# Kernel optimization log

Measured on AMD Instinct MI355X. Metric: run time of the kernel, lower is better.

## Reference

```python
import jax, jax.numpy as jnp
import numpy as np

CHEB_K = 3  # diffusion_steps

def setup_inputs() -> dict:
    key = jax.random.key(0)
    k1, k2, k3 = jax.random.split(key, 3)
    N, D, B, C, O, K = 2048, 16, 64, 64, 64, CHEB_K
    node_embeddings = jax.random.normal(k1, (N, D), dtype=jnp.float32)
    feat = jax.random.normal(k2, (B, N, C), dtype=jnp.float32)
    # kaiming-uniform-like init for weights_pool, zeros bias (matches reset_parameters)
    fan_in = K * C  # fan_in of [D, K, C, O] per torch convention (dims after first)
    bound = 1.0 / np.sqrt(fan_in)
    weights_pool = jax.random.uniform(k3, (D, K, C, O), dtype=jnp.float32,
                                      minval=-bound, maxval=bound)
    bias_pool = jnp.zeros((D, O), dtype=jnp.float32)
    return {"node_embeddings": node_embeddings, "feat": feat,
            "weights_pool": weights_pool, "bias_pool": bias_pool}

def reference(node_embeddings, feat, weights_pool, bias_pool):
    N = node_embeddings.shape[0]
    K = weights_pool.shape[1]
    # adaptive adjacency: softmax(relu(E E^T)) row-wise
    sim = node_embeddings @ node_embeddings.T            # [N, N]
    supports = jax.nn.softmax(jax.nn.relu(sim), axis=1)  # [N, N]
    # Chebyshev polynomial recurrence: T0=I, T1=A, Tk = 2A Tk-1 - Tk-2
    support_set = [jnp.eye(N, dtype=supports.dtype), supports]
    for _ in range(2, K):
        support_set.append(2.0 * supports @ support_set[-1] - support_set[-2])
    supports_k = jnp.stack(support_set, axis=0)          # [K, N, N]
    # node-conditioned weights and bias
    weights = jnp.einsum('nd,dkio->nkio', node_embeddings, weights_pool)  # [N,K,C,O]
    bias = node_embeddings @ bias_pool                                    # [N, O]
    # graph diffusion of features
    x_g = jnp.einsum('knm,bmc->bknc', supports_k, feat)  # [B, K, N, C]
    x_g = jnp.transpose(x_g, (0, 2, 1, 3))               # [B, N, K, C]
    # per-node batched GEMM + bias
    x_gconv = jnp.einsum('bnki,nkio->bno', x_g, weights) + bias
    return x_gconv
```

## Files before the change

### kernel.cpp

```cpp
#include <hip/hip_runtime.h>
#include <stdint.h>

#define NN 2048
#define DE 16
#define BB 64
#define CC 64
#define OO 64
#define BC 4096
#define KR 192

using bf16x8 = __attribute__((ext_vector_type(8))) __bf16;
using f32x4  = __attribute__((ext_vector_type(4))) float;

__device__ __forceinline__ unsigned short f2bf(float f) {
  union { float f; unsigned int u; } v; v.f = f;
  unsigned int u = v.u;
  return (unsigned short)((u + 0x7FFFu + ((u >> 16) & 1u)) >> 16);
}
__device__ __forceinline__ float bf2f(unsigned short h) {
  union { unsigned int u; float f; } v; v.u = ((unsigned int)h) << 16;
  return v.f;
}
__device__ __forceinline__ void gll16(const void* g, void* l) {
  __builtin_amdgcn_global_load_lds(
      (const __attribute__((address_space(1))) unsigned int*)g,
      (__attribute__((address_space(3))) unsigned int*)l, 16, 0, 0);
}

__global__ __launch_bounds__(256) void pack_feat(const float* __restrict__ feat,
                                                 unsigned short* __restrict__ Fbf,
                                                 unsigned short* __restrict__ FbfT) {
  __shared__ float tile[64][65];
  const int b  = blockIdx.y;
  const int n0 = blockIdx.x * 64;
  const int t  = threadIdx.x;
  const int tr = t >> 4, tc4 = (t & 15) * 4;
#pragma unroll
  for (int i = 0; i < 4; ++i) {
    const int r = tr + i * 16;
    const float4 v = *(const float4*)(feat + (size_t)b * (NN * CC) + (size_t)(n0 + r) * CC + tc4);
    tile[r][tc4 + 0] = v.x; tile[r][tc4 + 1] = v.y;
    tile[r][tc4 + 2] = v.z; tile[r][tc4 + 3] = v.w;
  }
  __syncthreads();
#pragma unroll
  for (int i = 0; i < 4; ++i) {
    const int r = tr + i * 16;
    const unsigned int lo = f2bf(tile[r][tc4 + 0]) | ((unsigned int)f2bf(tile[r][tc4 + 1]) << 16);
    const unsigned int hi = f2bf(tile[r][tc4 + 2]) | ((unsigned int)f2bf(tile[r][tc4 + 3]) << 16);
    *(uint2*)(Fbf + (size_t)(n0 + r) * BC + b * CC + tc4) = make_uint2(lo, hi);
  }
  const int rr = t & 63;
  const int cb = t >> 6;
#pragma unroll
  for (int i = 0; i < 16; ++i) {
    const int c = cb * 16 + i;
    FbfT[(size_t)(b * CC + c) * NN + n0 + rr] = f2bf(tile[rr][c]);
  }
}

__global__ __launch_bounds__(256) void adj_softmax(const float* __restrict__ E,
                                                   const float* __restrict__ bias_pool,
                                                   unsigned short* __restrict__ Abf,
                                                   float* __restrict__ Bias) {
  const int n = blockIdx.x, t = threadIdx.x;
  __shared__ float en[16];
  __shared__ float red[8];
  if (t < 16) en[t] = E[n * 16 + t];
  __syncthreads();
  float er[16];
#pragma unroll
  for (int d = 0; d < 16; ++d) er[d] = en[d];

  float v[8];
  float mx = 0.0f;
#pragma unroll
  for (int i = 0; i < 8; ++i) {
    const int m = t + i * 256;
    const float4* Em = (const float4*)(E + m * 16);
    const float4 a = Em[0], b = Em[1], c = Em[2], d = Em[3];
    float dot = er[0] * a.x + er[1] * a.y + er[2] * a.z + er[3] * a.w
              + er[4] * b.x + er[5] * b.y + er[6] * b.z + er[7] * b.w
              + er[8] * c.x + er[9] * c.y + er[10] * c.z + er[11] * c.w
              + er[12] * d.x + er[13] * d.y + er[14] * d.z + er[15] * d.w;
    v[i] = fmaxf(dot, 0.0f);
    mx = fmaxf(mx, v[i]);
  }
#pragma unroll
  for (int off = 32; off > 0; off >>= 1) mx = fmaxf(mx, __shfl_xor(mx, off, 64));
  const int wave = t >> 6, lane = t & 63;
  if (lane == 0) red[wave] = mx;
  __syncthreads();
  mx = fmaxf(fmaxf(red[0], red[1]), fmaxf(red[2], red[3]));
  float s = 0.0f;
#pragma unroll
  for (int i = 0; i < 8; ++i) { v[i] = __expf(v[i] - mx); s += v[i]; }
#pragma unroll
  for (int off = 32; off > 0; off >>= 1) s += __shfl_xor(s, off, 64);
  if (lane == 0) red[4 + wave] = s;
  __syncthreads();
  s = red[4] + red[5] + red[6] + red[7];
  const float inv = 1.0f / s;
#pragma unroll
  for (int i = 0; i < 8; ++i)
    Abf[(size_t)n * NN + t + i * 256] = f2bf(v[i] * inv);
  if (t < 64) {
    float bs = 0.0f;
#pragma unroll
    for (int d = 0; d < 16; ++d) bs += er[d] * bias_pool[d * 64 + t];
    Bias[n * 64 + t] = bs;
  }
}

__global__ __launch_bounds__(256) void make_w(const float* __restrict__ wp,
                                              const float* __restrict__ E,
                                              unsigned short* __restrict__ Wg) {
  __shared__ float wl[16][8][64];
  __shared__ float el[64][16];
  const int rq = blockIdx.x;
  const int n0 = blockIdx.y * 64;
  const int t  = threadIdx.x;
  for (int p = t; p < 2048; p += 256) {
    const int idx = p * 4;
    const int d = idx >> 9, rem = idx & 511, rl = rem >> 6, o = rem & 63;
    *(float4*)&wl[d][rl][o] = *(const float4*)(wp + (size_t)d * (KR * OO) + (size_t)(rq * 8 + rl) * 64 + o);
  }
  {
    const int nl = t >> 2, d4 = (t & 3) * 4;
    *(float4*)&el[nl][d4] = *(const float4*)(E + (size_t)(n0 + nl) * 16 + d4);
  }
  __syncthreads();
  const int o = t & 63, ng = t >> 6;
  for (int ii = 0; ii < 16; ++ii) {
    const int nl = ng * 16 + ii;
    float a[8] = {0, 0, 0, 0, 0, 0, 0, 0};
#pragma unroll
    for (int d = 0; d < 16; ++d) {
      const float e = el[nl][d];
#pragma unroll
      for (int rl = 0; rl < 8; ++rl) a[rl] = fmaf(e, wl[d][rl][o], a[rl]);
    }
    const unsigned int w0 = f2bf(a[0]) | ((unsigned int)f2bf(a[1]) << 16);
    const unsigned int w1 = f2bf(a[2]) | ((unsigned int)f2bf(a[3]) << 16);
    const unsigned int w2 = f2bf(a[4]) | ((unsigned int)f2bf(a[5]) << 16);
    const unsigned int w3 = f2bf(a[6]) | ((unsigned int)f2bf(a[7]) << 16);
    *(uint4*)(Wg + (size_t)(n0 + nl) * (KR * OO) + (size_t)rq * 512 + o * 8) =
        make_uint4(w0, w1, w2, w3);
  }
}

template <int EPI>
__global__ __launch_bounds__(256, 2) void gemm128(const unsigned short* __restrict__ A,
                                                  const unsigned short* __restrict__ Bt,
                                                  unsigned short* __restrict__ Cnm,
                                                  unsigned short* __restrict__ Ct,
                                                  const unsigned short* __restrict__ F) {
  __shared__ alignas(16) unsigned short As[128 * 32];
  __shared__ alignas(16) unsigned short Bs[128 * 32];
  const int t = threadIdx.x;
  const int bm = blockIdx.y * 128, bn = blockIdx.x * 128;
  const int wave = t >> 6, lane = t & 63;
  const int wm = (wave >> 1) * 64, wn = (wave & 1) * 64;

  f32x4 acc[4][4];
#pragma unroll
  for (int r = 0; r < 4; ++r)
#pragma unroll
    for (int c = 0; c < 4; ++c) acc[r][c] = (f32x4){0.f, 0.f, 0.f, 0.f};

  const int e0 = t * 8, e1 = (t + 256) * 8;
  const int r0 = e0 >> 5, c0 = e0 & 31;
  const int r1 = e1 >> 5, c1 = e1 & 31;
  const unsigned short* A0 = A + (size_t)(bm + r0) * NN + c0;
  const unsigned short* A1 = A + (size_t)(bm + r1) * NN + c1;
  const unsigned short* B0 = Bt + (size_t)(bn + r0) * NN + c0;
  const unsigned short* B1 = Bt + (size_t)(bn + r1) * NN + c1;
  const int aoff = (wm + (lane & 15)) * 32 + (lane >> 4) * 8;
  const int boff = (wn + (lane & 15)) * 32 + (lane >> 4) * 8;

  for (int k0 = 0; k0 < NN; k0 += 32) {
    __syncthreads();
    gll16(A0 + k0, &As[e0]);
    gll16(A1 + k0, &As[e1]);
    gll16(B0 + k0, &Bs[e0]);
    gll16(B1 + k0, &Bs[e1]);
    __syncthreads();
    bf16x8 af[4], bfr[4];
#pragma unroll
    for (int r = 0; r < 4; ++r) af[r] = *(const bf16x8*)&As[aoff + r * 512];
#pragma unroll
    for (int c = 0; c < 4; ++c) bfr[c] = *(const bf16x8*)&Bs[boff + c * 512];
#pragma unroll
    for (int r = 0; r < 4; ++r)
#pragma unroll
      for (int c = 0; c < 4; ++c)
        acc[r][c] = __builtin_amdgcn_mfma_f32_16x16x32_bf16(af[r], bfr[c], acc[r][c], 0, 0, 0);
  }

  const int colL = lane & 15, rowL = (lane >> 4) * 4;
#pragma unroll
  for (int r = 0; r < 4; ++r) {
#pragma unroll
    for (int c = 0; c < 4; ++c) {
      const int gm = bm + wm + r * 16 + rowL;
      const int gn = bn + wn + c * 16 + colL;
      const f32x4 a = acc[r][c];
      if (EPI == 1) {
#pragma unroll
        for (int i = 0; i < 4; ++i)
          Cnm[(size_t)(gm + i) * BC + gn] = f2bf(a[i]);
        const unsigned int lo = f2bf(a[0]) | ((unsigned int)f2bf(a[1]) << 16);
        const unsigned int hi = f2bf(a[2]) | ((unsigned int)f2bf(a[3]) << 16);
        *(uint2*)(Ct + (size_t)gn * NN + gm) = make_uint2(lo, hi);
      } else {
#pragma unroll
        for (int i = 0; i < 4; ++i) {
          const float g = 2.0f * a[i] - bf2f(F[(size_t)(gm + i) * BC + gn]);
          Cnm[(size_t)(gm + i) * BC + gn] = f2bf(g);
        }
      }
    }
  }
}

__global__ __launch_bounds__(256) void final_gemm(const unsigned short* __restrict__ Fbf,
                                                  const unsigned short* __restrict__ G1,
                                                  const unsigned short* __restrict__ G2,
                                                  const unsigned short* __restrict__ Wg,
                                                  const float* __restrict__ Bias,
                                                  float* __restrict__ out) {
  __shared__ alignas(16) unsigned short Xl[64 * 200];
  __shared__ alignas(16) unsigned short Wl[KR * OO];
  const int n = blockIdx.x, t = threadIdx.x;
  const unsigned short* srcs[3] = {Fbf + (size_t)n * BC, G1 + (size_t)n * BC, G2 + (size_t)n * BC};
#pragma unroll
  for (int kk = 0; kk < 3; ++kk) {
    const uint4* s = (const uint4*)srcs[kk];
    for (int p = t; p < 512; p += 256) {
      const uint4 v = s[p];
      const int j = p * 8, b = j >> 6, i = j & 63;
      *(uint4*)&Xl[b * 200 + kk * 64 + i] = v;
    }
  }
  {
    const uint4* s = (const uint4*)(Wg + (size_t)n * (KR * OO));
    uint4* d = (uint4*)Wl;
    for (int p = t; p < 1536; p += 256) d[p] = s[p];
  }
  __syncthreads();

  const int wave = t >> 6, lane = t & 63;
  const int q = lane >> 4;
  const int brow = wave * 16 + (lane & 15);
  f32x4 acc[4];
#pragma unroll
  for (int c = 0; c < 4; ++c) acc[c] = (f32x4){0.f, 0.f, 0.f, 0.f};
#pragma unroll
  for (int kq = 0; kq < 6; ++kq) {
    const bf16x8 a = *(const bf16x8*)&Xl[brow * 200 + kq * 32 + q * 8];
#pragma unroll
    for (int c = 0; c < 4; ++c) {
      const bf16x8 b = *(const bf16x8*)&Wl[(kq * 4 + q) * 512 + (c * 16 + (lane & 15)) * 8];
      acc[c] = __builtin_amdgcn_mfma_f32_16x16x32_bf16(a, b, acc[c], 0, 0, 0);
    }
  }
  const int col = lane & 15, rbase = wave * 16 + q * 4;
#pragma unroll
  for (int c = 0; c < 4; ++c) {
    const int o = c * 16 + col;
    const float bs = Bias[n * 64 + o];
#pragma unroll
    for (int i = 0; i < 4; ++i)
      out[(size_t)(rbase + i) * (NN * OO) + (size_t)n * OO + o] = acc[c][i] + bs;
  }
}

extern "C" void kernel_launch(void* const* d_in, const int* in_sizes, int n_in,
                              void* d_out, int out_size, void* d_ws, size_t ws_size,
                              hipStream_t stream) {
  const float* E    = (const float*)d_in[0];
  const float* feat = (const float*)d_in[1];
  const float* wp   = (const float*)d_in[2];
  const float* bp   = (const float*)d_in[3];
  float* out = (float*)d_out;

  char* ws = (char*)d_ws;
  size_t off = 0;
  auto alloc = [&](size_t bytes) -> void* {
    void* p = ws + off;
    off += (bytes + 255) & ~(size_t)255;
    return p;
  };
  unsigned short* Abf  = (unsigned short*)alloc((size_t)NN * NN * 2);
  unsigned short* FbfT = (unsigned short*)alloc((size_t)BC * NN * 2);
  unsigned short* Fbf  = (unsigned short*)alloc((size_t)NN * BC * 2);
  unsigned short* G1   = (unsigned short*)alloc((size_t)NN * BC * 2);
  unsigned short* G1T  = (unsigned short*)alloc((size_t)BC * NN * 2);
  unsigned short* Wg   = (unsigned short*)alloc((size_t)NN * KR * OO * 2);
  float* Bias          = (float*)alloc((size_t)NN * OO * 4);
  unsigned short* G2   = FbfT;

  pack_feat<<<dim3(32, 64), 256, 0, stream>>>(feat, Fbf, FbfT);
  adj_softmax<<<dim3(2048), 256, 0, stream>>>(E, bp, Abf, Bias);
  make_w<<<dim3(24, 32), 256, 0, stream>>>(wp, E, Wg);
  gemm128<1><<<dim3(32, 16), 256, 0, stream>>>(Abf, FbfT, G1, G1T, nullptr);
  gemm128<2><<<dim3(32, 16), 256, 0, stream>>>(Abf, G1T, G2, nullptr, Fbf);
  final_gemm<<<dim3(2048), 256, 0, stream>>>(Fbf, G1, G2, Wg, Bias, out);
}
```

Before: 256.6 us.

## Merge prep kernels into one launch, restructure weight gen, swizzle GEMM LDS

Combines the feature pack, adjacency softmax and per-node weight generation into a single block-indexed prep kernel, so two launches and their tail gaps go away. Weight generation now keeps the pool weights in registers and streams node embeddings through scalar loads instead of staging both in shared memory. Separately, the GEMM LDS tiles use an XOR swizzle on the 8-element column chunk to reduce bank conflicts on fragment reads. The fused kernel's occupancy is bounded by its largest branch's shared memory and register use, and the weight branch holds a 64-float register array.

Measured after the change: 239.7 us. -6.6%, faster.

```diff
diff --git a/kernel.cpp b/kernel.cpp
--- a/kernel.cpp
+++ b/kernel.cpp
@@ -27,125 +27,124 @@
       (__attribute__((address_space(3))) unsigned int*)l, 16, 0, 0);
 }
 
-__global__ __launch_bounds__(256) void pack_feat(const float* __restrict__ feat,
-                                                 unsigned short* __restrict__ Fbf,
-                                                 unsigned short* __restrict__ FbfT) {
-  __shared__ float tile[64][65];
-  const int b  = blockIdx.y;
-  const int n0 = blockIdx.x * 64;
+__global__ __launch_bounds__(256) void prep(const float* __restrict__ feat,
+                                            const float* __restrict__ E,
+                                            const float* __restrict__ wp,
+                                            const float* __restrict__ bp,
+                                            unsigned short* __restrict__ Fbf,
+                                            unsigned short* __restrict__ FbfT,
+                                            unsigned short* __restrict__ Abf,
+                                            float* __restrict__ Bias,
+                                            unsigned short* __restrict__ Wg) {
+  __shared__ float smem[64 * 65];
+  const int id = blockIdx.x;
   const int t  = threadIdx.x;
-  const int tr = t >> 4, tc4 = (t & 15) * 4;
-#pragma unroll
-  for (int i = 0; i < 4; ++i) {
-    const int r = tr + i * 16;
-    const float4 v = *(const float4*)(feat + (size_t)b * (NN * CC) + (size_t)(n0 + r) * CC + tc4);
-    tile[r][tc4 + 0] = v.x; tile[r][tc4 + 1] = v.y;
-    tile[r][tc4 + 2] = v.z; tile[r][tc4 + 3] = v.w;
-  }
-  __syncthreads();
-#pragma unroll
-  for (int i = 0; i < 4; ++i) {
-    const int r = tr + i * 16;
-    const unsigned int lo = f2bf(tile[r][tc4 + 0]) | ((unsigned int)f2bf(tile[r][tc4 + 1]) << 16);
-    const unsigned int hi = f2bf(tile[r][tc4 + 2]) | ((unsigned int)f2bf(tile[r][tc4 + 3]) << 16);
-    *(uint2*)(Fbf + (size_t)(n0 + r) * BC + b * CC + tc4) = make_uint2(lo, hi);
-  }
-  const int rr = t & 63;
-  const int cb = t >> 6;
-#pragma unroll
-  for (int i = 0; i < 16; ++i) {
-    const int c = cb * 16 + i;
-    FbfT[(size_t)(b * CC + c) * NN + n0 + rr] = f2bf(tile[rr][c]);
-  }
-}
-
-__global__ __launch_bounds__(256) void adj_softmax(const float* __restrict__ E,
-                                                   const float* __restrict__ bias_pool,
-                                                   unsigned short* __restrict__ Abf,
-                                                   float* __restrict__ Bias) {
-  const int n = blockIdx.x, t = threadIdx.x;
-  __shared__ float en[16];
-  __shared__ float red[8];
-  if (t < 16) en[t] = E[n * 16 + t];
-  __syncthreads();
-  float er[16];
-#pragma unroll
-  for (int d = 0; d < 16; ++d) er[d] = en[d];
-
-  float v[8];
-  float mx = 0.0f;
-#pragma unroll
-  for (int i = 0; i < 8; ++i) {
-    const int m = t + i * 256;
-    const float4* Em = (const float4*)(E + m * 16);
-    const float4 a = Em[0], b = Em[1], c = Em[2], d = Em[3];
-    float dot = er[0] * a.x + er[1] * a.y + er[2] * a.z + er[3] * a.w
-              + er[4] * b.x + er[5] * b.y + er[6] * b.z + er[7] * b.w
-              + er[8] * c.x + er[9] * c.y + er[10] * c.z + er[11] * c.w
-              + er[12] * d.x + er[13] * d.y + er[14] * d.z + er[15] * d.w;
-    v[i] = fmaxf(dot, 0.0f);
-    mx = fmaxf(mx, v[i]);
-  }
-#pragma unroll
-  for (int off = 32; off > 0; off >>= 1) mx = fmaxf(mx, __shfl_xor(mx, off, 64));
-  const int wave = t >> 6, lane = t & 63;
-  if (lane == 0) red[wave] = mx;
-  __syncthreads();
-  mx = fmaxf(fmaxf(red[0], red[1]), fmaxf(red[2], red[3]));
-  float s = 0.0f;
-#pragma unroll
-  for (int i = 0; i < 8; ++i) { v[i] = __expf(v[i] - mx); s += v[i]; }
-#pragma unroll
-  for (int off = 32; off > 0; off >>= 1) s += __shfl_xor(s, off, 64);
-  if (lane == 0) red[4 + wave] = s;
-  __syncthreads();
-  s = red[4] + red[5] + red[6] + red[7];
-  const float inv = 1.0f / s;
-#pragma unroll
-  for (int i = 0; i < 8; ++i)
-    Abf[(size_t)n * NN + t + i * 256] = f2bf(v[i] * inv);
-  if (t < 64) {
-    float bs = 0.0f;
-#pragma unroll
-    for (int d = 0; d < 16; ++d) bs += er[d] * bias_pool[d * 64 + t];
-    Bias[n * 64 + t] = bs;
-  }
-}
-
-__global__ __launch_bounds__(256) void make_w(const float* __restrict__ wp,
-                                              const float* __restrict__ E,
-                                              unsigned short* __restrict__ Wg) {
-  __shared__ float wl[16][8][64];
-  __shared__ float el[64][16];
-  const int rq = blockIdx.x;
-  const int n0 = blockIdx.y * 64;
-  const int t  = threadIdx.x;
-  for (int p = t; p < 2048; p += 256) {
-    const int idx = p * 4;
-    const int d = idx >> 9, rem = idx & 511, rl = rem >> 6, o = rem & 63;
-    *(float4*)&wl[d][rl][o] = *(const float4*)(wp + (size_t)d * (KR * OO) + (size_t)(rq * 8 + rl) * 64 + o);
-  }
-  {
-    const int nl = t >> 2, d4 = (t & 3) * 4;
-    *(float4*)&el[nl][d4] = *(const float4*)(E + (size_t)(n0 + nl) * 16 + d4);
-  }
-  __syncthreads();
-  const int o = t & 63, ng = t >> 6;
-  for (int ii = 0; ii < 16; ++ii) {
-    const int nl = ng * 16 + ii;
-    float a[8] = {0, 0, 0, 0, 0, 0, 0, 0};
-#pragma unroll
-    for (int d = 0; d < 16; ++d) {
-      const float e = el[nl][d];
-#pragma unroll
-      for (int rl = 0; rl < 8; ++rl) a[rl] = fmaf(e, wl[d][rl][o], a[rl]);
-    }
-    const unsigned int w0 = f2bf(a[0]) | ((unsigned int)f2bf(a[1]) << 16);
-    const unsigned int w1 = f2bf(a[2]) | ((unsigned int)f2bf(a[3]) << 16);
-    const unsigned int w2 = f2bf(a[4]) | ((unsigned int)f2bf(a[5]) << 16);
-    const unsigned int w3 = f2bf(a[6]) | ((unsigned int)f2bf(a[7]) << 16);
-    *(uint4*)(Wg + (size_t)(n0 + nl) * (KR * OO) + (size_t)rq * 512 + o * 8) =
-        make_uint4(w0, w1, w2, w3);
+
+  if (id < 2048) {
+    float (*tile)[65] = (float (*)[65])smem;
+    const int b  = id >> 5;
+    const int n0 = (id & 31) * 64;
+    const int tr = t >> 4, tc4 = (t & 15) * 4;
+#pragma unroll
+    for (int i = 0; i < 4; ++i) {
+      const int r = tr + i * 16;
+      const float4 v = *(const float4*)(feat + (size_t)b * (NN * CC) + (size_t)(n0 + r) * CC + tc4);
+      tile[r][tc4 + 0] = v.x; tile[r][tc4 + 1] = v.y;
+      tile[r][tc4 + 2] = v.z; tile[r][tc4 + 3] = v.w;
+    }
+    __syncthreads();
+#pragma unroll
+    for (int i = 0; i < 4; ++i) {
+      const int r = tr + i * 16;
+      const unsigned int lo = f2bf(tile[r][tc4 + 0]) | ((unsigned int)f2bf(tile[r][tc4 + 1]) << 16);
+      const unsigned int hi = f2bf(tile[r][tc4 + 2]) | ((unsigned int)f2bf(tile[r][tc4 + 3]) << 16);
+      *(uint2*)(Fbf + (size_t)(n0 + r) * BC + b * CC + tc4) = make_uint2(lo, hi);
+    }
+    const int rr = t & 63;
+    const int cb = t >> 6;
+#pragma unroll
+    for (int i = 0; i < 16; ++i) {
+      const int c = cb * 16 + i;
+      FbfT[(size_t)(b * CC + c) * NN + n0 + rr] = f2bf(tile[rr][c]);
+    }
+  } else if (id < 4096) {
+    const int n = id - 2048;
+    float* en  = smem;
+    float* red = smem + 16;
+    if (t < 16) en[t] = E[n * 16 + t];
+    __syncthreads();
+    float er[16];
+#pragma unroll
+    for (int d = 0; d < 16; ++d) er[d] = en[d];
+
+    float v[8];
+    float mx = 0.0f;
+#pragma unroll
+    for (int i = 0; i < 8; ++i) {
+      const int m = t + i * 256;
+      const float4* Em = (const float4*)(E + m * 16);
+      const float4 a = Em[0], b = Em[1], c = Em[2], d = Em[3];
+      float dot = er[0] * a.x + er[1] * a.y + er[2] * a.z + er[3] * a.w
+                + er[4] * b.x + er[5] * b.y + er[6] * b.z + er[7] * b.w
+                + er[8] * c.x + er[9] * c.y + er[10] * c.z + er[11] * c.w
+                + er[12] * d.x + er[13] * d.y + er[14] * d.z + er[15] * d.w;
+      v[i] = fmaxf(dot, 0.0f);
+      mx = fmaxf(mx, v[i]);
+    }
+#pragma unroll
+    for (int off = 32; off > 0; off >>= 1) mx = fmaxf(mx, __shfl_xor(mx, off, 64));
+    const int wave = t >> 6, lane = t & 63;
+    if (lane == 0) red[wave] = mx;
+    __syncthreads();
+    mx = fmaxf(fmaxf(red[0], red[1]), fmaxf(red[2], red[3]));
+    float s = 0.0f;
+#pragma unroll
+    for (int i = 0; i < 8; ++i) { v[i] = __expf(v[i] - mx); s += v[i]; }
+#pragma unroll
+    for (int off = 32; off > 0; off >>= 1) s += __shfl_xor(s, off, 64);
+    if (lane == 0) red[4 + wave] = s;
+    __syncthreads();
+    s = red[4] + red[5] + red[6] + red[7];
+    const float inv = 1.0f / s;
+#pragma unroll
+    for (int i = 0; i < 8; ++i)
+      Abf[(size_t)n * NN + t + i * 256] = f2bf(v[i] * inv);
+    if (t < 64) {
+      float bs = 0.0f;
+#pragma unroll
+      for (int d = 0; d < 16; ++d) bs += er[d] * bp[d * 64 + t];
+      Bias[n * 64 + t] = bs;
+    }
+  } else {
+    const int wid = id - 4096;
+    const int rq = wid % 24;
+    const int nc = wid / 24;
+    const int o  = t & 63;
+    const int rh = (t >> 6) & 1;
+    const int g  = t >> 7;
+    float w[16][4];
+#pragma unroll
+    for (int d = 0; d < 16; ++d)
+#pragma unroll
+      for (int j = 0; j < 4; ++j)
+        w[d][j] = wp[(size_t)d * (KR * OO) + (size_t)(rq * 8 + rh * 4 + j) * 64 + o];
+    const int nbase = nc * 128 + g * 64;
+    for (int i = 0; i < 64; ++i) {
+      const int ns = __builtin_amdgcn_readfirstlane(nbase + i);
+      const float* ep = E + ns * 16;
+      float a0 = 0.f, a1 = 0.f, a2 = 0.f, a3 = 0.f;
+#pragma unroll
+      for (int d = 0; d < 16; ++d) {
+        const float e = ep[d];
+        a0 = fmaf(e, w[d][0], a0);
+        a1 = fmaf(e, w[d][1], a1);
+        a2 = fmaf(e, w[d][2], a2);
+        a3 = fmaf(e, w[d][3], a3);
+      }
+      const unsigned int lo = f2bf(a0) | ((unsigned int)f2bf(a1) << 16);
+      const unsigned int hi = f2bf(a2) | ((unsigned int)f2bf(a3) << 16);
+      *(uint2*)(Wg + (size_t)ns * (KR * OO) + rq * 512 + o * 8 + rh * 4) = make_uint2(lo, hi);
+    }
   }
 }
 
@@ -168,15 +167,17 @@
 #pragma unroll
     for (int c = 0; c < 4; ++c) acc[r][c] = (f32x4){0.f, 0.f, 0.f, 0.f};
 
+  const int r0 = t >> 2;
+  const int csw = (((t & 3) ^ ((r0 >> 1) & 3)) * 8);
+  const unsigned short* A0 = A + (size_t)(bm + r0) * NN + csw;
+  const unsigned short* A1 = A + (size_t)(bm + r0 + 64) * NN + csw;
+  const unsigned short* B0 = Bt + (size_t)(bn + r0) * NN + csw;
+  const unsigned short* B1 = Bt + (size_t)(bn + r0 + 64) * NN + csw;
   const int e0 = t * 8, e1 = (t + 256) * 8;
-  const int r0 = e0 >> 5, c0 = e0 & 31;
-  const int r1 = e1 >> 5, c1 = e1 & 31;
-  const unsigned short* A0 = A + (size_t)(bm + r0) * NN + c0;
-  const unsigned short* A1 = A + (size_t)(bm + r1) * NN + c1;
-  const unsigned short* B0 = Bt + (size_t)(bn + r0) * NN + c0;
-  const unsigned short* B1 = Bt + (size_t)(bn + r1) * NN + c1;
-  const int aoff = (wm + (lane & 15)) * 32 + (lane >> 4) * 8;
-  const int boff = (wn + (lane & 15)) * 32 + (lane >> 4) * 8;
+
+  const int li = lane & 15, q = lane >> 4, sw = (li >> 1) & 3;
+  const int aoff = (wm + li) * 32 + ((q ^ sw) * 8);
+  const int boff = (wn + li) * 32 + ((q ^ sw) * 8);
 
   for (int k0 = 0; k0 < NN; k0 += 32) {
     __syncthreads();
@@ -300,9 +301,7 @@
   float* Bias          = (float*)alloc((size_t)NN * OO * 4);
   unsigned short* G2   = FbfT;
 
-  pack_feat<<<dim3(32, 64), 256, 0, stream>>>(feat, Fbf, FbfT);
-  adj_softmax<<<dim3(2048), 256, 0, stream>>>(E, bp, Abf, Bias);
-  make_w<<<dim3(24, 32), 256, 0, stream>>>(wp, E, Wg);
+  prep<<<dim3(4480), 256, 0, stream>>>(feat, E, wp, bp, Fbf, FbfT, Abf, Bias, Wg);
   gemm128<1><<<dim3(32, 16), 256, 0, stream>>>(Abf, FbfT, G1, G1T, nullptr);
   gemm128<2><<<dim3(32, 16), 256, 0, stream>>>(Abf, G1T, G2, nullptr, Fbf);
   final_gemm<<<dim3(2048), 256, 0, stream>>>(Fbf, G1, G2, Wg, Bias, out);
```
